# Kernel optimization log

Hardware: AMD Instinct MI355X
Metric: run time of the kernel (lower is better)

## Reference

```python
import jax, jax.numpy as jnp
import numpy as np

# --- static config matching init_kwargs ---
PATTERN_SPECS = {4: 25, 5: 25, 6: 25, 7: 25}
P = sum(PATTERN_SPECS.values())          # total_num_patterns = 100
MAXL = max(PATTERN_SPECS.keys())          # max_pattern_length = 7
D = 300                                   # embedding_dim
V = 10000                                 # local vocab size
B = 32                                    # batch size
T = 2048                                  # max_doc_len
NC = 2                                    # num_classes
BIAS_SCALE = 1.0
EPS = 1e-5
TAU = 0.0
# end state per pattern (pattern_len - 1), ordered by pattern_specs
END_IDX = np.array([l - 1 for l, n in PATTERN_SPECS.items() for _ in range(n)], dtype=np.int32)


def setup_inputs() -> dict:
    key = jax.random.key(0)
    ks = jax.random.split(key, 8)
    local_embeddings = jax.random.normal(ks[0], (D, V), jnp.float32)
    diags = jax.random.normal(ks[1], (P * (MAXL - 1), D), jnp.float32) * (2.0 / (P * (MAXL - 1) + D)) ** 0.5
    bias = jax.random.normal(ks[2], (P * (MAXL - 1), 1), jnp.float32) * 0.05
    wildcards = jax.random.normal(ks[3], (P, MAXL - 1), jnp.float32) * 0.1
    linear_w = jax.random.normal(ks[4], (NC, P), jnp.float32) * 0.1
    linear_b = jnp.zeros((NC,), jnp.float32)
    docs = jax.random.randint(ks[5], (B, T), 0, V)
    doc_lens = jax.random.randint(ks[6], (B,), T // 2, T + 1)
    return dict(local_embeddings=local_embeddings, diags=diags, bias=bias,
                wildcards=wildcards, linear_w=linear_w, linear_b=linear_b,
                docs=docs, doc_lens=doc_lens)


def masked_layer_norm(x, eps=EPS):
    # MaskedLayerNorm with mask = ~isinf(x); equals plain layer_norm when no infs.
    mask = ~jnp.isinf(x)
    masked = jnp.where(mask, x, 0.0)
    divisor = jnp.sum(mask, axis=1, keepdims=True).astype(x.dtype)
    mean = jnp.sum(masked, axis=1, keepdims=True) / divisor
    var = jnp.sum(jnp.where(mask, (masked - mean) ** 2, 0.0), axis=1, keepdims=True) / divisor
    normalized = (masked - mean) / jnp.sqrt(var + eps)
    return jnp.where(mask, normalized, x)


def reference(local_embeddings, diags, bias, wildcards, linear_w, linear_b, docs, doc_lens):
    # MaxSum semiring: zero=-inf, one=0, plus=max, times=+, identity outer maps.
    # transition scores per local token: [V, P*(MAXL-1)] -> gather per doc token
    trans = (diags @ local_embeddings + BIAS_SCALE * bias).T          # [V, P*(L-1)]
    tm = trans[docs].reshape(B, T, P, MAXL - 1)                        # [B,T,P,L-1]
    wc = wildcards[None]                                               # wildcard_scale = semiring.one = 0
    end_idx = jnp.asarray(END_IDX)
    pidx = jnp.arange(P)

    restart = jnp.zeros((B, P, 1), tm.dtype)                           # semiring.one
    h0 = jnp.concatenate([restart, jnp.full((B, P, MAXL - 1), -jnp.inf, tm.dtype)], axis=2)
    s0 = jnp.full((B, P), -jnp.inf, tm.dtype)                          # semiring.zero
    tm_seq = jnp.moveaxis(tm, 1, 0)                                    # [T,B,P,L-1]

    def step(carry, inp):
        scores, hiddens = carry
        tmt, t = inp
        prev = hiddens[:, :, :-1]                                      # [B,P,L-1]
        main = jnp.concatenate([restart, prev + tmt], axis=2)          # semiring.times
        wild = jnp.concatenate([restart, prev + wc], axis=2)
        hiddens = jnp.maximum(main, wild)                              # semiring.plus
        end_vals = hiddens[:, pidx, end_idx]                           # gather end states [B,P]
        active = (doc_lens > t)[:, None]
        scores = jnp.where(active, jnp.maximum(scores, end_vals), scores)
        return (scores, hiddens), None

    (scores, _), _ = jax.lax.scan(step, (s0, h0), (tm_seq, jnp.arange(T)))

    scores = masked_layer_norm(scores)
    scores = (scores > TAU).astype(scores.dtype)                       # STE binarizer (forward)
    return scores @ linear_w.T + linear_b
```

## Files before the change

### kernel.cpp

```cpp
#include <hip/hip_runtime.h>
#include <hip/hip_bf16.h>
#include <cmath>
#include <cstdint>

#define V_   10000
#define D_   300
#define P_   100
#define B_   32
#define T_   2048
#define NC_  2
#define CP_  450
#define CPAD 464

__device__ __constant__ int PS_[9] = {0, 13, 26, 38, 51, 63, 76, 88, 100};

__device__ __forceinline__ int maprow(int c) {
    if (c < 75)  return (c / 3) * 6 + c % 3;
    if (c < 175) { int q = c - 75;  return (25 + q / 4) * 6 + q % 4; }
    if (c < 300) { int q = c - 175; return (50 + q / 5) * 6 + q % 5; }
    int q = c - 300; return (75 + q / 6) * 6 + q % 6;
}
__device__ __forceinline__ int cstart(int p) {
    if (p < 25) return 3 * p;
    if (p < 50) return 75 + 4 * (p - 25);
    if (p < 75) return 175 + 5 * (p - 50);
    return 300 + 6 * (p - 75);
}
__device__ __forceinline__ uint32_t fkey(float v) {
    uint32_t u = __float_as_uint(v);
    return (u & 0x80000000u) ? ~u : (u | 0x80000000u);
}
__device__ __forceinline__ float fdec(uint32_t k) {
    uint32_t u = (k & 0x80000000u) ? (k ^ 0x80000000u) : ~k;
    return __uint_as_float(u);
}

__device__ __forceinline__ void load_lds16(const float* g, float* l) {
    __builtin_amdgcn_global_load_lds((const __attribute__((address_space(1))) void*)g,
                                     (__attribute__((address_space(3))) void*)l, 16, 0, 0);
}

__global__ __launch_bounds__(256) void k_tr(const float* __restrict__ diags,
                                            const float* __restrict__ bias,
                                            const float* __restrict__ wc,
                                            float* __restrict__ dT,
                                            float* __restrict__ bp,
                                            float* __restrict__ wp,
                                            uint32_t* __restrict__ scoresU) {
    const int idx = blockIdx.x * 256 + threadIdx.x;
    if (idx < B_ * P_) scoresU[idx] = 0x007FFFFFu;
    if (idx < CPAD) {
        float b = 0.f, w = 0.f;
        if (idx < CP_) { int r = maprow(idx); b = bias[r]; w = wc[r]; }
        bp[idx] = b; wp[idx] = w;
    }
    if (idx < D_ * CPAD) {
        const int d = idx / CPAD, cp = idx - d * CPAD;
        dT[idx] = (cp < CP_) ? diags[maprow(cp) * D_ + d] : 0.f;
    }
}

__global__ __launch_bounds__(256) void k_gemm(const float* __restrict__ emb,
                                              const float* __restrict__ dT,
                                              const float* __restrict__ bp,
                                              const float* __restrict__ wp,
                                              float* __restrict__ mt) {
    __shared__ __align__(16) float embT[2][10][512];
    const int bid = blockIdx.x;
    const int xcd = bid & 7, ii = bid >> 3;
    const int ord = (xcd < 4) ? (xcd * 73 + ii) : (292 + (xcd - 4) * 72 + ii);
    const int vt = ord / 29, ct = ord - vt * 29;
    const int v0 = vt * 512, c0 = ct * 16;

    const int tid  = threadIdx.x;
    const int lane = tid & 63;
    const int wid  = tid >> 6;
    const int widv = wid & 1;
    const int cb   = __builtin_amdgcn_readfirstlane(c0 + (wid >> 1) * 8);

    float acc[4][8] = {};

    auto stage = [&](int buf, int d0) {
        for (int r = wid; r < 10; r += 4) {
            #pragma unroll
            for (int h = 0; h < 2; ++h) {
                int vsrc = v0 + h * 256 + (lane << 2);
                vsrc = min(vsrc, V_ - 4);
                load_lds16(emb + (size_t)(d0 + r) * V_ + vsrc, &embT[buf][r][h * 256]);
            }
        }
    };

    stage(0, 0);
    __syncthreads();

    for (int ch = 0; ch < 30; ++ch) {
        if (ch < 29) stage((ch + 1) & 1, (ch + 1) * 10);
        const int buf = ch & 1;
        #pragma unroll
        for (int dd = 0; dd < 10; ++dd) {
            const float4 ev = *(const float4*)&embT[buf][dd][widv * 256 + (lane << 2)];
            const float* dr = dT + (size_t)(ch * 10 + dd) * CPAD + cb;
            float dg[8];
            #pragma unroll
            for (int j = 0; j < 8; ++j) dg[j] = dr[j];
            const float evf[4] = {ev.x, ev.y, ev.z, ev.w};
            #pragma unroll
            for (int i4 = 0; i4 < 4; ++i4)
                #pragma unroll
                for (int j = 0; j < 8; ++j)
                    acc[i4][j] = fmaf(evf[i4], dg[j], acc[i4][j]);
        }
        __syncthreads();
    }

    float bs[8], ws2[8];
    #pragma unroll
    for (int j = 0; j < 8; ++j) { bs[j] = bp[cb + j]; ws2[j] = wp[cb + j]; }
    const int vb = v0 + widv * 256 + (lane << 2);
    #pragma unroll
    for (int i4 = 0; i4 < 4; ++i4) {
        const int v = vb + i4;
        if (v < V_) {
            float4 o0, o1;
            o0.x = fmaxf(acc[i4][0] + bs[0], ws2[0]);
            o0.y = fmaxf(acc[i4][1] + bs[1], ws2[1]);
            o0.z = fmaxf(acc[i4][2] + bs[2], ws2[2]);
            o0.w = fmaxf(acc[i4][3] + bs[3], ws2[3]);
            o1.x = fmaxf(acc[i4][4] + bs[4], ws2[4]);
            o1.y = fmaxf(acc[i4][5] + bs[5], ws2[5]);
            o1.z = fmaxf(acc[i4][6] + bs[6], ws2[6]);
            o1.w = fmaxf(acc[i4][7] + bs[7], ws2[7]);
            *(float4*)&mt[(size_t)v * CPAD + cb]     = o0;
            *(float4*)&mt[(size_t)v * CPAD + cb + 4] = o1;
        }
    }
}

__global__ __launch_bounds__(256) void k_scan(const float* __restrict__ mt,
                                              const int* __restrict__ docs,
                                              const int* __restrict__ doc_lens,
                                              uint32_t* __restrict__ scoresU) {
    __shared__ float sm[37][453];
    __shared__ int rowbuf[37];
    const int bid = blockIdx.x;
    const int b = bid & 31, ts = bid >> 5;
    const int ts0 = ts * 32;
    const int tid = threadIdx.x;
    const int lane = tid & 63, wid = tid >> 6;
    const int len = doc_lens[b];
    const int nst = min(37, T_ - ts0);

    for (int q = tid; q < nst; q += 256) rowbuf[q] = docs[b * T_ + ts0 + q];
    __syncthreads();
    for (int r = wid; r < nst; r += 4) {
        const float* src = mt + (size_t)rowbuf[r] * CPAD;
        load_lds16(src + (lane << 2), &sm[r][0]);
        if (lane < 49) load_lds16(src + 256 + (lane << 2), &sm[r][256]);
    }
    __syncthreads();

    const int t = tid & 31;
    const int pset = tid >> 5;
    const int p0 = PS_[pset], p1 = PS_[pset + 1];
    for (int p = p0; p < p1; ++p) {
        const int e = 3 + p / 25;
        const int cb = cstart(p);
        float s = sm[t][cb];
        for (int i2 = 1; i2 < e; ++i2) s += sm[t + i2][cb + i2];
        float val = (ts0 + t + e <= len) ? s : -INFINITY;
        #pragma unroll
        for (int off = 16; off > 0; off >>= 1)
            val = fmaxf(val, __shfl_xor(val, off, 32));
        if (t == 0) atomicMax(&scoresU[b * P_ + p], fkey(val));
    }
}

__global__ __launch_bounds__(128) void k_final(const uint32_t* __restrict__ scoresU,
                                               const float* __restrict__ lw,
                                               const float* __restrict__ lb,
                                               float* __restrict__ out) {
    const int b = blockIdx.x;
    const int tid = threadIdx.x;
    __shared__ float sh[P_];
    __shared__ float stats[2];

    float s = 0.f;
    bool fin = false;
    if (tid < P_) {
        s = fdec(scoresU[b * P_ + tid]);
        fin = !isinf(s);
        sh[tid] = s;
    }
    __syncthreads();
    if (tid == 0) {
        int n = 0; float sum = 0.f;
        for (int p = 0; p < P_; p++) {
            float x = sh[p];
            if (!isinf(x)) { n++; sum += x; }
        }
        float mean = sum / (float)n;
        float var = 0.f;
        for (int p = 0; p < P_; p++) {
            float x = sh[p];
            if (!isinf(x)) { float d = x - mean; var += d * d; }
        }
        var /= (float)n;
        stats[0] = mean;
        stats[1] = 1.f / sqrtf(var + 1e-5f);
    }
    __syncthreads();
    if (tid < P_) {
        float norm = fin ? (s - stats[0]) * stats[1] : s;
        sh[tid] = (norm > 0.f) ? 1.f : 0.f;
    }
    __syncthreads();
    if (tid < NC_) {
        float accv = lb[tid];
        for (int p = 0; p < P_; p++) accv += sh[p] * lw[tid * P_ + p];
        out[b * NC_ + tid] = accv;
    }
}

extern "C" void kernel_launch(void* const* d_in, const int* in_sizes, int n_in,
                              void* d_out, int out_size, void* d_ws, size_t ws_size,
                              hipStream_t stream) {
    const float* emb   = (const float*)d_in[0];
    const float* diags = (const float*)d_in[1];
    const float* bias  = (const float*)d_in[2];
    const float* wc    = (const float*)d_in[3];
    const float* lw    = (const float*)d_in[4];
    const float* lb    = (const float*)d_in[5];
    const int*   docs  = (const int*)d_in[6];
    const int*   dlens = (const int*)d_in[7];
    float* out = (float*)d_out;

    float*    mt      = (float*)d_ws;
    float*    dT      = mt + (size_t)V_ * CPAD;
    float*    bp      = dT + (size_t)D_ * CPAD;
    float*    wp      = bp + CPAD;
    uint32_t* scoresU = (uint32_t*)(wp + CPAD);

    k_tr   <<<dim3(544),  256, 0, stream>>>(diags, bias, wc, dT, bp, wp, scoresU);
    k_gemm <<<dim3(580),  256, 0, stream>>>(emb, dT, bp, wp, mt);
    k_scan <<<dim3(2048), 256, 0, stream>>>(mt, docs, dlens, scoresU);
    k_final<<<dim3(B_),   128, 0, stream>>>(scoresU, lw, lb, out);
}
```

Baseline: 180.5 us.

## Retile transition GEMM to 8-column tiles, trim padding, skip scan blocks past doc length

The transition-score GEMM is retiled so each block covers 512 vocab rows by 8 columns, with each thread doing 2x8 outputs instead of 4x8. This doubles the grid to 1140 blocks and sets an occupancy hint of 4. The column padding shrinks from 464 to 456, which cuts the size of the mt table written and gathered. The scan kernel now returns early for time tiles that start beyond the document length and loads only the rows it needs. The cost is that each embedding tile is reused across fewer columns, so the same embedding data is reloaded by more blocks.

```diff
diff --git a/kernel.cpp b/kernel.cpp
--- a/kernel.cpp
+++ b/kernel.cpp
@@ -10,7 +10,7 @@
 #define T_   2048
 #define NC_  2
 #define CP_  450
-#define CPAD 464
+#define CPAD 456
 
 __device__ __constant__ int PS_[9] = {0, 13, 26, 38, 51, 63, 76, 88, 100};
 
@@ -60,34 +60,33 @@
     }
 }
 
-__global__ __launch_bounds__(256) void k_gemm(const float* __restrict__ emb,
-                                              const float* __restrict__ dT,
-                                              const float* __restrict__ bp,
-                                              const float* __restrict__ wp,
-                                              float* __restrict__ mt) {
+__global__ __launch_bounds__(256, 4) void k_gemm(const float* __restrict__ emb,
+                                                 const float* __restrict__ dT,
+                                                 const float* __restrict__ bp,
+                                                 const float* __restrict__ wp,
+                                                 float* __restrict__ mt) {
     __shared__ __align__(16) float embT[2][10][512];
     const int bid = blockIdx.x;
     const int xcd = bid & 7, ii = bid >> 3;
-    const int ord = (xcd < 4) ? (xcd * 73 + ii) : (292 + (xcd - 4) * 72 + ii);
-    const int vt = ord / 29, ct = ord - vt * 29;
-    const int v0 = vt * 512, c0 = ct * 16;
+    const int ord = (xcd < 4) ? (xcd * 143 + ii) : (572 + (xcd - 4) * 142 + ii);
+    const int vt = ord / 57, ct = ord - vt * 57;
+    const int v0 = vt * 512;
+    const int cb = __builtin_amdgcn_readfirstlane(ct * 8);
 
     const int tid  = threadIdx.x;
     const int lane = tid & 63;
     const int wid  = tid >> 6;
-    const int widv = wid & 1;
-    const int cb   = __builtin_amdgcn_readfirstlane(c0 + (wid >> 1) * 8);
-
-    float acc[4][8] = {};
+
+    float acc[2][8] = {};
 
     auto stage = [&](int buf, int d0) {
-        for (int r = wid; r < 10; r += 4) {
-            #pragma unroll
-            for (int h = 0; h < 2; ++h) {
-                int vsrc = v0 + h * 256 + (lane << 2);
-                vsrc = min(vsrc, V_ - 4);
-                load_lds16(emb + (size_t)(d0 + r) * V_ + vsrc, &embT[buf][r][h * 256]);
-            }
+        #pragma unroll
+        for (int k = 0; k < 5; ++k) {
+            const int u = wid + (k << 2);
+            const int r = u >> 1, hf = u & 1;
+            int vsrc = v0 + (hf << 8) + (lane << 2);
+            vsrc = min(vsrc, V_ - 4);
+            load_lds16(emb + (size_t)(d0 + r) * V_ + vsrc, &embT[buf][r][hf << 8]);
         }
     };
 
@@ -99,17 +98,16 @@
         const int buf = ch & 1;
         #pragma unroll
         for (int dd = 0; dd < 10; ++dd) {
-            const float4 ev = *(const float4*)&embT[buf][dd][widv * 256 + (lane << 2)];
+            const float2 ev = *(const float2*)&embT[buf][dd][(wid << 7) + (lane << 1)];
             const float* dr = dT + (size_t)(ch * 10 + dd) * CPAD + cb;
             float dg[8];
             #pragma unroll
             for (int j = 0; j < 8; ++j) dg[j] = dr[j];
-            const float evf[4] = {ev.x, ev.y, ev.z, ev.w};
             #pragma unroll
-            for (int i4 = 0; i4 < 4; ++i4)
-                #pragma unroll
-                for (int j = 0; j < 8; ++j)
-                    acc[i4][j] = fmaf(evf[i4], dg[j], acc[i4][j]);
+            for (int j = 0; j < 8; ++j) {
+                acc[0][j] = fmaf(ev.x, dg[j], acc[0][j]);
+                acc[1][j] = fmaf(ev.y, dg[j], acc[1][j]);
+            }
         }
         __syncthreads();
     }
@@ -117,20 +115,20 @@
     float bs[8], ws2[8];
     #pragma unroll
     for (int j = 0; j < 8; ++j) { bs[j] = bp[cb + j]; ws2[j] = wp[cb + j]; }
-    const int vb = v0 + widv * 256 + (lane << 2);
+    const int vbase = v0 + (wid << 7) + (lane << 1);
     #pragma unroll
-    for (int i4 = 0; i4 < 4; ++i4) {
-        const int v = vb + i4;
+    for (int i2 = 0; i2 < 2; ++i2) {
+        const int v = vbase + i2;
         if (v < V_) {
             float4 o0, o1;
-            o0.x = fmaxf(acc[i4][0] + bs[0], ws2[0]);
-            o0.y = fmaxf(acc[i4][1] + bs[1], ws2[1]);
-            o0.z = fmaxf(acc[i4][2] + bs[2], ws2[2]);
-            o0.w = fmaxf(acc[i4][3] + bs[3], ws2[3]);
-            o1.x = fmaxf(acc[i4][4] + bs[4], ws2[4]);
-            o1.y = fmaxf(acc[i4][5] + bs[5], ws2[5]);
-            o1.z = fmaxf(acc[i4][6] + bs[6], ws2[6]);
-            o1.w = fmaxf(acc[i4][7] + bs[7], ws2[7]);
+            o0.x = fmaxf(acc[i2][0] + bs[0], ws2[0]);
+            o0.y = fmaxf(acc[i2][1] + bs[1], ws2[1]);
+            o0.z = fmaxf(acc[i2][2] + bs[2], ws2[2]);
+            o0.w = fmaxf(acc[i2][3] + bs[3], ws2[3]);
+            o1.x = fmaxf(acc[i2][4] + bs[4], ws2[4]);
+            o1.y = fmaxf(acc[i2][5] + bs[5], ws2[5]);
+            o1.z = fmaxf(acc[i2][6] + bs[6], ws2[6]);
+            o1.w = fmaxf(acc[i2][7] + bs[7], ws2[7]);
             *(float4*)&mt[(size_t)v * CPAD + cb]     = o0;
             *(float4*)&mt[(size_t)v * CPAD + cb + 4] = o1;
         }
@@ -146,10 +144,11 @@
     const int bid = blockIdx.x;
     const int b = bid & 31, ts = bid >> 5;
     const int ts0 = ts * 32;
+    const int len = doc_lens[b];
+    if (ts0 + 3 > len) return;
     const int tid = threadIdx.x;
     const int lane = tid & 63, wid = tid >> 6;
-    const int len = doc_lens[b];
-    const int nst = min(37, T_ - ts0);
+    const int nst = min(min(37, T_ - ts0), len - ts0);
 
     for (int q = tid; q < nst; q += 256) rowbuf[q] = docs[b * T_ + ts0 + q];
     __syncthreads();
@@ -241,8 +240,8 @@
     float*    wp      = bp + CPAD;
     uint32_t* scoresU = (uint32_t*)(wp + CPAD);
 
-    k_tr   <<<dim3(544),  256, 0, stream>>>(diags, bias, wc, dT, bp, wp, scoresU);
-    k_gemm <<<dim3(580),  256, 0, stream>>>(emb, dT, bp, wp, mt);
+    k_tr   <<<dim3(535),  256, 0, stream>>>(diags, bias, wc, dT, bp, wp, scoresU);
+    k_gemm <<<dim3(1140), 256, 0, stream>>>(emb, dT, bp, wp, mt);
     k_scan <<<dim3(2048), 256, 0, stream>>>(mt, docs, dlens, scoresU);
     k_final<<<dim3(B_),   128, 0, stream>>>(scoresU, lw, lb, out);
 }
```

Measured after the change: 189.7 us. 1.05x slower.

## Simplify GEMM to per-thread vocab rows and split scan by pattern groups

Applied to the files above, without the earlier changes.

The GEMM kernel drops its double-buffered LDS staging. Each thread now computes one vocab row by 16 columns, reading embeddings directly from global memory, and the grid doubles to 1160 blocks. The scan kernel is restructured so that each block covers 64 timesteps and one of four pattern-column groups, loading only a 128-column slice of each transition row into LDS. Blocks that fall past the document length exit early. This is meant to cut LDS and global traffic in the scan, at the risk of lower data reuse in the simpler GEMM.

```diff
diff --git a/kernel.cpp b/kernel.cpp
--- a/kernel.cpp
+++ b/kernel.cpp
@@ -12,7 +12,8 @@
 #define CP_  450
 #define CPAD 464
 
-__device__ __constant__ int PS_[9] = {0, 13, 26, 38, 51, 63, 76, 88, 100};
+__device__ __constant__ int G_c0[4] = {0, 124, 240, 348};
+__device__ __constant__ int G_p0[5] = {0, 38, 63, 83, 100};
 
 __device__ __forceinline__ int maprow(int c) {
     if (c < 75)  return (c / 3) * 6 + c % 3;
@@ -65,114 +66,79 @@
                                               const float* __restrict__ bp,
                                               const float* __restrict__ wp,
                                               float* __restrict__ mt) {
-    __shared__ __align__(16) float embT[2][10][512];
     const int bid = blockIdx.x;
     const int xcd = bid & 7, ii = bid >> 3;
-    const int ord = (xcd < 4) ? (xcd * 73 + ii) : (292 + (xcd - 4) * 72 + ii);
+    const int ord = xcd * 145 + ii;
     const int vt = ord / 29, ct = ord - vt * 29;
-    const int v0 = vt * 512, c0 = ct * 16;
-
-    const int tid  = threadIdx.x;
-    const int lane = tid & 63;
-    const int wid  = tid >> 6;
-    const int widv = wid & 1;
-    const int cb   = __builtin_amdgcn_readfirstlane(c0 + (wid >> 1) * 8);
-
-    float acc[4][8] = {};
-
-    auto stage = [&](int buf, int d0) {
-        for (int r = wid; r < 10; r += 4) {
-            #pragma unroll
-            for (int h = 0; h < 2; ++h) {
-                int vsrc = v0 + h * 256 + (lane << 2);
-                vsrc = min(vsrc, V_ - 4);
-                load_lds16(emb + (size_t)(d0 + r) * V_ + vsrc, &embT[buf][r][h * 256]);
-            }
-        }
-    };
-
-    stage(0, 0);
-    __syncthreads();
-
-    for (int ch = 0; ch < 30; ++ch) {
-        if (ch < 29) stage((ch + 1) & 1, (ch + 1) * 10);
-        const int buf = ch & 1;
-        #pragma unroll
-        for (int dd = 0; dd < 10; ++dd) {
-            const float4 ev = *(const float4*)&embT[buf][dd][widv * 256 + (lane << 2)];
-            const float* dr = dT + (size_t)(ch * 10 + dd) * CPAD + cb;
-            float dg[8];
-            #pragma unroll
-            for (int j = 0; j < 8; ++j) dg[j] = dr[j];
-            const float evf[4] = {ev.x, ev.y, ev.z, ev.w};
-            #pragma unroll
-            for (int i4 = 0; i4 < 4; ++i4)
-                #pragma unroll
-                for (int j = 0; j < 8; ++j)
-                    acc[i4][j] = fmaf(evf[i4], dg[j], acc[i4][j]);
-        }
-        __syncthreads();
-    }
-
-    float bs[8], ws2[8];
-    #pragma unroll
-    for (int j = 0; j < 8; ++j) { bs[j] = bp[cb + j]; ws2[j] = wp[cb + j]; }
-    const int vb = v0 + widv * 256 + (lane << 2);
-    #pragma unroll
-    for (int i4 = 0; i4 < 4; ++i4) {
-        const int v = vb + i4;
-        if (v < V_) {
-            float4 o0, o1;
-            o0.x = fmaxf(acc[i4][0] + bs[0], ws2[0]);
-            o0.y = fmaxf(acc[i4][1] + bs[1], ws2[1]);
-            o0.z = fmaxf(acc[i4][2] + bs[2], ws2[2]);
-            o0.w = fmaxf(acc[i4][3] + bs[3], ws2[3]);
-            o1.x = fmaxf(acc[i4][4] + bs[4], ws2[4]);
-            o1.y = fmaxf(acc[i4][5] + bs[5], ws2[5]);
-            o1.z = fmaxf(acc[i4][6] + bs[6], ws2[6]);
-            o1.w = fmaxf(acc[i4][7] + bs[7], ws2[7]);
-            *(float4*)&mt[(size_t)v * CPAD + cb]     = o0;
-            *(float4*)&mt[(size_t)v * CPAD + cb + 4] = o1;
-        }
-    }
-}
+    const int cb = ct * 16;
+    const int tid = threadIdx.x;
+    const int v = vt * 256 + tid;
+    const int vc = min(v, V_ - 1);
+
+    const float* ep = emb + vc;
+    const float* dr = dT + cb;
+
+    float acc[16] = {};
+    #pragma unroll 2
+    for (int d = 0; d < D_; ++d) {
+        const float ev = ep[(size_t)d * V_];
+        const float* dg = dr + (size_t)d * CPAD;
+        #pragma unroll
+        for (int j = 0; j < 16; ++j)
+            acc[j] = fmaf(ev, dg[j], acc[j]);
+    }
+
+    if (v < V_) {
+        #pragma unroll
+        for (int j = 0; j < 16; ++j)
+            acc[j] = fmaxf(acc[j] + bp[cb + j], wp[cb + j]);
+        float* op = mt + (size_t)v * CPAD + cb;
+        #pragma unroll
+        for (int q = 0; q < 4; ++q)
+            *(float4*)(op + q * 4) = make_float4(acc[q*4], acc[q*4+1],
+                                                 acc[q*4+2], acc[q*4+3]);
+    }
+}
+
+#define SROW 69
+#define SST  132
 
 __global__ __launch_bounds__(256) void k_scan(const float* __restrict__ mt,
                                               const int* __restrict__ docs,
                                               const int* __restrict__ doc_lens,
                                               uint32_t* __restrict__ scoresU) {
-    __shared__ float sm[37][453];
-    __shared__ int rowbuf[37];
+    __shared__ float sm[SROW][SST];
+    __shared__ int rowbuf[SROW];
     const int bid = blockIdx.x;
-    const int b = bid & 31, ts = bid >> 5;
-    const int ts0 = ts * 32;
+    const int pg = bid & 3;
+    const int ts = (bid >> 2) & 31;
+    const int b  = bid >> 7;
+    const int ts0 = ts * 64;
+    const int len = doc_lens[b];
+    if (ts0 + 3 > len) return;
     const int tid = threadIdx.x;
     const int lane = tid & 63, wid = tid >> 6;
-    const int len = doc_lens[b];
-    const int nst = min(37, T_ - ts0);
+    const int nst = min(SROW, min(T_ - ts0, len - ts0));
+    const int c0 = G_c0[pg];
 
     for (int q = tid; q < nst; q += 256) rowbuf[q] = docs[b * T_ + ts0 + q];
     __syncthreads();
-    for (int r = wid; r < nst; r += 4) {
-        const float* src = mt + (size_t)rowbuf[r] * CPAD;
-        load_lds16(src + (lane << 2), &sm[r][0]);
-        if (lane < 49) load_lds16(src + 256 + (lane << 2), &sm[r][256]);
-    }
-    __syncthreads();
-
-    const int t = tid & 31;
-    const int pset = tid >> 5;
-    const int p0 = PS_[pset], p1 = PS_[pset + 1];
-    for (int p = p0; p < p1; ++p) {
+    for (int r = wid; r < nst; r += 4)
+        if (lane < 32)
+            load_lds16(mt + (size_t)rowbuf[r] * CPAD + c0 + (lane << 2), &sm[r][0]);
+    __syncthreads();
+
+    const int t = lane;
+    for (int p = G_p0[pg] + wid; p < G_p0[pg + 1]; p += 4) {
         const int e = 3 + p / 25;
-        const int cb = cstart(p);
-        float s = sm[t][cb];
-        for (int i2 = 1; i2 < e; ++i2) s += sm[t + i2][cb + i2];
+        const int cbs = cstart(p) - c0;
+        float s = sm[t][cbs];
+        for (int i = 1; i < e; ++i) s += sm[t + i][cbs + i];
         float val = (ts0 + t + e <= len) ? s : -INFINITY;
         #pragma unroll
-        for (int off = 16; off > 0; off >>= 1)
-            val = fmaxf(val, __shfl_xor(val, off, 32));
-        if (t == 0) atomicMax(&scoresU[b * P_ + p], fkey(val));
+        for (int off = 32; off > 0; off >>= 1)
+            val = fmaxf(val, __shfl_xor(val, off, 64));
+        if (lane == 0) atomicMax(&scoresU[b * P_ + p], fkey(val));
     }
 }
 
@@ -242,7 +208,7 @@
     uint32_t* scoresU = (uint32_t*)(wp + CPAD);
 
     k_tr   <<<dim3(544),  256, 0, stream>>>(diags, bias, wc, dT, bp, wp, scoresU);
-    k_gemm <<<dim3(580),  256, 0, stream>>>(emb, dT, bp, wp, mt);
-    k_scan <<<dim3(2048), 256, 0, stream>>>(mt, docs, dlens, scoresU);
+    k_gemm <<<dim3(1160), 256, 0, stream>>>(emb, dT, bp, wp, mt);
+    k_scan <<<dim3(4096), 256, 0, stream>>>(mt, docs, dlens, scoresU);
     k_final<<<dim3(B_),   128, 0, stream>>>(scoresU, lw, lb, out);
 }
```

After: 184.8 us. 1.02x slower.
